# Kernel optimization log

Measured on AMD Instinct MI355X. Metric: run time of the kernel, lower is better.

The kernel has to match this reference:

```python
import jax, jax.numpy as jnp
import numpy as np

EPS_BN = 1e-5
EPS_LN = 1e-5


def conv2d(x, w, stride=1, padding=0):
    # x: [B,C,H,W], w: [O,I,kh,kw]
    return jax.lax.conv_general_dilated(
        x, w, (stride, stride), [(padding, padding), (padding, padding)],
        dimension_numbers=("NCHW", "OIHW", "NCHW"))


def bn_relu(x, g, b, m, v):
    inv = g / jnp.sqrt(v + EPS_BN)
    return jax.nn.relu(x * inv[None, :, None, None] + (b - m * inv)[None, :, None, None])


def haar_dwt(x):
    # orthonormal 2D Haar: [B,C,H,W] -> [B,4C,H/2,W/2] as concat(LL,LH,HL,HH)
    B, C, H, W = x.shape
    x = x.reshape(B, C, H // 2, 2, W // 2, 2)
    a = x[:, :, :, 0, :, 0]; b = x[:, :, :, 0, :, 1]
    c = x[:, :, :, 1, :, 0]; d = x[:, :, :, 1, :, 1]
    ll = (a + b + c + d) * 0.5
    lh = (a - b + c - d) * 0.5
    hl = (a + b - c - d) * 0.5
    hh = (a - b - c + d) * 0.5
    return jnp.concatenate([ll, lh, hl, hh], axis=1)


def haar_idwt(co):
    # exact inverse of haar_dwt: [B,4C,h,w] -> [B,C,2h,2w]
    B, C4, h, w = co.shape
    ll, lh, hl, hh = jnp.split(co, 4, axis=1)
    a = (ll + lh + hl + hh) * 0.5
    b = (ll - lh + hl - hh) * 0.5
    c = (ll + lh - hl - hh) * 0.5
    d = (ll - lh - hl + hh) * 0.5
    row0 = jnp.stack([a, b], axis=-1)  # [B,C,h,w,2]
    row1 = jnp.stack([c, d], axis=-1)
    y = jnp.stack([row0, row1], axis=3)  # [B,C,h,2,w,2]
    return y.reshape(B, C4 // 4, 2 * h, 2 * w)


def layernorm(x, g, b):
    mu = jnp.mean(x, axis=-1, keepdims=True)
    var = jnp.mean(jnp.square(x - mu), axis=-1, keepdims=True)
    return (x - mu) * jax.lax.rsqrt(var + EPS_LN) * g + b


def setup_inputs() -> dict:
    key = jax.random.key(0)
    ks = jax.random.split(key, 20)
    B, N, C = 16, 3136, 256
    red = C // 4  # 64
    sr = 2
    d = {}
    d["x"] = jax.random.normal(ks[0], (B, N, C), jnp.float32)
    d["height"] = 56
    d["width"] = 56
    # reduce: conv1x1 C->red (no bias) + BN
    d["reduce_w"] = jax.random.normal(ks[1], (red, C, 1, 1), jnp.float32) * 0.05
    d["bn1_g"] = jax.random.uniform(ks[2], (red,), jnp.float32, 0.5, 1.5)
    d["bn1_b"] = jax.random.normal(ks[3], (red,), jnp.float32) * 0.1
    d["bn1_m"] = jax.random.normal(ks[4], (red,), jnp.float32) * 0.1
    d["bn1_v"] = jax.random.uniform(ks[5], (red,), jnp.float32, 0.5, 1.5)
    # filter: conv3x3 C->C (no bias) + BN  (acts on 4*red = C coeff channels)
    d["filt_w"] = jax.random.normal(ks[6], (C, C, 3, 3), jnp.float32) * 0.02
    d["bn2_g"] = jax.random.uniform(ks[7], (C,), jnp.float32, 0.5, 1.5)
    d["bn2_b"] = jax.random.normal(ks[8], (C,), jnp.float32) * 0.1
    d["bn2_m"] = jax.random.normal(ks[9], (C,), jnp.float32) * 0.1
    d["bn2_v"] = jax.random.uniform(ks[10], (C,), jnp.float32, 0.5, 1.5)
    # kv_embed: conv kxk stride sr, C->C, with bias
    d["kve_w"] = jax.random.normal(ks[11], (C, C, sr, sr), jnp.float32) * 0.05
    d["kve_b"] = jnp.zeros((C,), jnp.float32)
    # q linear
    d["q_w"] = jax.random.normal(ks[12], (C, C), jnp.float32) * 0.05
    d["q_b"] = jnp.zeros((C,), jnp.float32)
    # kv layernorm + kv linear
    d["kvn_g"] = jnp.ones((C,), jnp.float32)
    d["kvn_b"] = jnp.zeros((C,), jnp.float32)
    d["kv_w"] = jax.random.normal(ks[13], (2 * C, C), jnp.float32) * 0.05
    d["kv_b"] = jnp.zeros((2 * C,), jnp.float32)
    # proj: (C + red) -> C
    d["proj_w"] = jax.random.normal(ks[14], (C, C + red), jnp.float32) * 0.05
    d["proj_b"] = jnp.zeros((C,), jnp.float32)
    return d


def reference(x, q_w, q_b, reduce_w, bn1_g, bn1_b, bn1_m, bn1_v,
              filt_w, bn2_g, bn2_b, bn2_m, bn2_v, kve_w, kve_b,
              kvn_g, kvn_b, kv_w, kv_b, proj_w, proj_b, height, width):
    B, N, C = x.shape
    H_heads, sr = 8, 2
    hd = C // H_heads
    scale = hd ** -0.5

    # queries [B,h,N,hd]
    q = (x @ q_w.T + q_b).reshape(B, N, H_heads, hd).transpose(0, 2, 1, 3)

    # spatial path
    spatial = x.transpose(0, 2, 1).reshape(B, C, height, width)
    reduced = bn_relu(conv2d(spatial, reduce_w), bn1_g, bn1_b, bn1_m, bn1_v)  # [B,C/4,H,W]
    coeffs = haar_dwt(reduced)  # [B,C,H/2,W/2]
    coeffs = bn_relu(conv2d(coeffs, filt_w, padding=1), bn2_g, bn2_b, bn2_m, bn2_v)
    local_context = haar_idwt(coeffs)  # [B,C/4,H,W]
    local_context = local_context.reshape(B, C // 4, N).transpose(0, 2, 1)  # [B,N,C/4]

    # kv path
    kv_src = conv2d(coeffs, kve_w, stride=sr) + kve_b[None, :, None, None]
    Bk, Ck, hk, wk = kv_src.shape
    kv_src = kv_src.reshape(B, C, hk * wk).transpose(0, 2, 1)  # [B,M,C]
    kv_src = layernorm(kv_src, kvn_g, kvn_b)
    kv = (kv_src @ kv_w.T + kv_b).reshape(B, -1, 2, H_heads, hd)
    kv = kv.transpose(2, 0, 3, 1, 4)  # [2,B,h,M,hd]
    key, value = kv[0], kv[1]

    # attention
    scores = jnp.einsum("bhnd,bhmd->bhnm", q, key) * scale
    probs = jax.nn.softmax(scores, axis=-1)
    attended = jnp.einsum("bhnm,bhmd->bhnd", probs, value)
    attended = attended.transpose(0, 2, 1, 3).reshape(B, N, C)

    out = jnp.concatenate([attended, local_context], axis=-1) @ proj_w.T + proj_b
    return out
```

## Files before the change

### kernel.cpp

```cpp
#include <hip/hip_runtime.h>
#include <hip/hip_bf16.h>
#include <math.h>


#define B_   16
#define NSP  3136
#define KVL  196
#define HD   32

typedef short bf16x8 __attribute__((ext_vector_type(8)));
typedef float f32x4  __attribute__((ext_vector_type(4)));

__device__ inline unsigned int f2bf(float f) {
    unsigned int u = __float_as_uint(f);
    u += 0x7FFFu + ((u >> 16) & 1u);
    return u >> 16;
}
__device__ inline float bf2f(unsigned short u) {
    return __uint_as_float(((unsigned int)u) << 16);
}
__device__ inline f32x4 max4(f32x4 a, f32x4 b) {
    f32x4 r;
    r[0] = fmaxf(a[0], b[0]); r[1] = fmaxf(a[1], b[1]);
    r[2] = fmaxf(a[2], b[2]); r[3] = fmaxf(a[3], b[3]);
    return r;
}

__global__ __launch_bounds__(256) void wcvt_k(
    const float* __restrict__ q, const float* __restrict__ red,
    const float* __restrict__ kv, const float* __restrict__ proj,
    unsigned short* __restrict__ dst)
{
    const int i = blockIdx.x * 256 + threadIdx.x;
    const int e = i * 4;
    const float* src; int off;
    if (e < 65536)       { src = q;    off = e; }
    else if (e < 81920)  { src = red;  off = e - 65536; }
    else if (e < 212992) { src = kv;   off = e - 81920; }
    else                 { src = proj; off = e - 212992; }
    const float4 v = *(const float4*)(src + off);
    const unsigned int p0 = f2bf(v.x) | (f2bf(v.y) << 16);
    const unsigned int p1 = f2bf(v.z) | (f2bf(v.w) << 16);
    *(uint2*)(dst + e) = make_uint2(p0, p1);
}

__global__ __launch_bounds__(256) void wcvt2_k(const float* __restrict__ kve,
                                               unsigned short* __restrict__ wk)
{
    const int i = blockIdx.x * 256 + threadIdx.x;
    const int n = i >> 8;
    const int rem = i & 255;
    const int tap = rem >> 6;
    const int ci0 = (rem & 63) * 4;
    const float* s = kve + (size_t)n * 1024;
    const unsigned int t0 = f2bf(s[(ci0 + 0) * 4 + tap]);
    const unsigned int t1 = f2bf(s[(ci0 + 1) * 4 + tap]);
    const unsigned int t2 = f2bf(s[(ci0 + 2) * 4 + tap]);
    const unsigned int t3 = f2bf(s[(ci0 + 3) * 4 + tap]);
    *(uint2*)(wk + (size_t)n * 1024 + tap * 256 + ci0) =
        make_uint2(t0 | (t1 << 16), t2 | (t3 << 16));
}

__global__ __launch_bounds__(256) void wcvt3_k(const float* __restrict__ filt,
                                               unsigned short* __restrict__ wf)
{
    const int i = blockIdx.x * 256 + threadIdx.x;
    const int n = i / 576;
    const int rem = (i - n * 576) * 4;
    const int tap = rem >> 8;
    const int ci = rem & 255;
    const float* s = filt + (size_t)n * 2304;
    const unsigned int t0 = f2bf(s[(ci + 0) * 9 + tap]);
    const unsigned int t1 = f2bf(s[(ci + 1) * 9 + tap]);
    const unsigned int t2 = f2bf(s[(ci + 2) * 9 + tap]);
    const unsigned int t3 = f2bf(s[(ci + 3) * 9 + tap]);
    *(uint2*)(wf + (size_t)n * 2304 + rem) = make_uint2(t0 | (t1 << 16), t2 | (t3 << 16));
}

template<int BM, int BN, int EPI, int LDM>
__global__ __launch_bounds__(256) void mgemm(
    const unsigned short* __restrict__ A, const float* __restrict__ Af,
    const unsigned short* __restrict__ Acl,
    const unsigned short* __restrict__ W, const float* __restrict__ bias,
    const float* __restrict__ g, const float* __restrict__ bb,
    const float* __restrict__ mm, const float* __restrict__ vv,
    float* __restrict__ out, float* __restrict__ out2,
    int Mpad, int Mvalid, int N, int K, float scale)
{
    constexpr int FM = BM / 32, FN = BN / 32;
    constexpr int RA = BM / 64, RB = BN / 64;
    __shared__ short As[BM][32];
    __shared__ short Bs[BN][32];
    const int tid = threadIdx.x, lane = tid & 63;
    const int w = tid >> 6, wr = w >> 1, wc = w & 1;
    const int b = blockIdx.z, m0 = blockIdx.x * BM, n0 = blockIdx.y * BN;
    const unsigned short* Ab = A + ((size_t)b * Mpad + m0) * (size_t)K;
    const unsigned short* Wb = W + (size_t)n0 * K;

    const int r_row0 = tid >> 2, kbase = (tid & 3) * 8;
    int ym[RA], xm[RA], mg[RA];
#pragma unroll
    for (int rnd = 0; rnd < RA; ++rnd) {
        const int m = m0 + rnd * 64 + r_row0;
        mg[rnd] = m;
        if constexpr (LDM == 1) { ym[rnd] = m / 28; xm[rnd] = m - 28 * ym[rnd]; }
        else if constexpr (LDM == 3) { ym[rnd] = m / 14; xm[rnd] = m - 14 * ym[rnd]; }
        else { ym[rnd] = 0; xm[rnd] = 0; }
    }

    f32x4 acc[FM][FN];
#pragma unroll
    for (int i = 0; i < FM; ++i)
#pragma unroll
        for (int j = 0; j < FN; ++j) acc[i][j] = (f32x4){0.f, 0.f, 0.f, 0.f};

    for (int k0 = 0; k0 < K; k0 += 32) {
#pragma unroll
        for (int rnd = 0; rnd < RA; ++rnd) {
            const int row = rnd * 64 + r_row0;
            if constexpr (LDM == 0) {
                *(int4*)&As[row][kbase] =
                    *(const int4*)(Ab + (size_t)row * K + k0 + kbase);
            } else if constexpr (LDM == 2) {
                unsigned int p0 = 0, p1 = 0, p2 = 0, p3 = 0;
                if (mg[rnd] < Mvalid) {
                    const float* sp = Af + ((size_t)b * Mvalid + mg[rnd]) * K + k0 + kbase;
                    const float4 v0 = *(const float4*)sp;
                    const float4 v1 = *(const float4*)(sp + 4);
                    p0 = f2bf(v0.x) | (f2bf(v0.y) << 16);
                    p1 = f2bf(v0.z) | (f2bf(v0.w) << 16);
                    p2 = f2bf(v1.x) | (f2bf(v1.y) << 16);
                    p3 = f2bf(v1.z) | (f2bf(v1.w) << 16);
                }
                *(int4*)&As[row][kbase] = make_int4(p0, p1, p2, p3);
            } else if constexpr (LDM == 1) {
                const int kk = k0 + kbase;
                const int tap = kk >> 8, ci0 = kk & 255;
                const int ky = tap / 3, kx = tap - 3 * ky;
                const int sy = ym[rnd] + ky - 1, sx = xm[rnd] + kx - 1;
                int4 v = make_int4(0, 0, 0, 0);
                if (mg[rnd] < Mvalid && sy >= 0 && sy < 28 && sx >= 0 && sx < 28)
                    v = *(const int4*)(Acl + ((size_t)b * 784 + sy * 28 + sx) * 256 + ci0);
                *(int4*)&As[row][kbase] = v;
            } else {
                const int kk = k0 + kbase;
                const int tap = kk >> 8, ci0 = kk & 255;
                const int ky = tap >> 1, kx = tap & 1;
                const int sy = 2 * ym[rnd] + ky, sx = 2 * xm[rnd] + kx;
                int4 v = make_int4(0, 0, 0, 0);
                if (mg[rnd] < Mvalid)
                    v = *(const int4*)(Acl + ((size_t)b * 784 + sy * 28 + sx) * 256 + ci0);
                *(int4*)&As[row][kbase] = v;
            }
        }
#pragma unroll
        for (int rnd = 0; rnd < RB; ++rnd) {
            const int row = rnd * 64 + r_row0;
            *(int4*)&Bs[row][kbase] =
                *(const int4*)(Wb + (size_t)row * K + k0 + kbase);
        }
        __syncthreads();
        bf16x8 af[FM], bfr[FN];
#pragma unroll
        for (int i = 0; i < FM; ++i)
            af[i] = *(const bf16x8*)&As[wr * (BM / 2) + i * 16 + (lane & 15)][(lane >> 4) * 8];
#pragma unroll
        for (int j = 0; j < FN; ++j)
            bfr[j] = *(const bf16x8*)&Bs[wc * (BN / 2) + j * 16 + (lane & 15)][(lane >> 4) * 8];
#pragma unroll
        for (int i = 0; i < FM; ++i)
#pragma unroll
            for (int j = 0; j < FN; ++j)
                acc[i][j] = __builtin_amdgcn_mfma_f32_16x16x32_bf16(af[i], bfr[j], acc[i][j], 0, 0, 0);
        __syncthreads();
    }

    const int cl = lane & 15, rh = lane >> 4;
#pragma unroll
    for (int i = 0; i < FM; ++i) {
#pragma unroll
        for (int j = 0; j < FN; ++j) {
            const int n = n0 + wc * (BN / 2) + j * 16 + cl;
#pragma unroll
            for (int r = 0; r < 4; ++r) {
                const int m = m0 + wr * (BM / 2) + i * 16 + rh * 4 + r;
                if (m >= Mvalid) continue;
                const float v = acc[i][j][r];
                if constexpr (EPI == 0) {
                    out[((size_t)b * Mvalid + m) * N + n] = v + bias[n];
                } else if constexpr (EPI == 1) {
                    unsigned short* qp = (unsigned short*)out;
                    const int h = (n >> 5) & 7, d = n & 31;
                    qp[(((size_t)b * 8 + h) * 3136 + m) * 32 + d] =
                        (unsigned short)f2bf((v + bias[n]) * scale);
                } else if constexpr (EPI == 3) {
                    const float val = v + bias[n];
                    const int h = (n >> 5) & 7, d = n & 31;
                    if (n < 256)
                        ((unsigned short*)out)[(((size_t)b * 8 + h) * 224 + m) * 32 + d] =
                            (unsigned short)f2bf(val);
                    else
                        ((unsigned short*)out2)[(((size_t)b * 8 + h) * 32 + d) * 224 + m] =
                            (unsigned short)f2bf(val);
                } else {
                    const float inv = g[n] * rsqrtf(vv[n] + 1e-5f);
                    const float rr = v * inv + (bb[n] - mm[n] * inv);
                    ((unsigned short*)out)[((size_t)b * Mvalid + m) * N + n] =
                        (unsigned short)f2bf(rr > 0.f ? rr : 0.f);
                }
            }
        }
    }
}

__global__ __launch_bounds__(256) void dwt_k(const unsigned short* __restrict__ rd,
                                             unsigned short* __restrict__ ccl)
{
    const int i = blockIdx.x * 256 + threadIdx.x;
    const int c4 = (i & 15) * 4;
    const int p = i >> 4;
    const int x = p % 28, y = (p / 28) % 28, b = p / 784;
    const unsigned short* ip = rd + ((size_t)b * 3136 + (2 * y) * 56 + 2 * x) * 64 + c4;
    const uint2 u00 = *(const uint2*)(ip);
    const uint2 u01 = *(const uint2*)(ip + 64);
    const uint2 u10 = *(const uint2*)(ip + 56 * 64);
    const uint2 u11 = *(const uint2*)(ip + 57 * 64);
    const unsigned short* s00 = (const unsigned short*)&u00;
    const unsigned short* s01 = (const unsigned short*)&u01;
    const unsigned short* s10 = (const unsigned short*)&u10;
    const unsigned short* s11 = (const unsigned short*)&u11;
    unsigned short ll[4], lh[4], hl[4], hh[4];
#pragma unroll
    for (int j = 0; j < 4; ++j) {
        const float a = bf2f(s00[j]), bq = bf2f(s01[j]);
        const float c = bf2f(s10[j]), d = bf2f(s11[j]);
        ll[j] = (unsigned short)f2bf((a + bq + c + d) * 0.5f);
        lh[j] = (unsigned short)f2bf((a - bq + c - d) * 0.5f);
        hl[j] = (unsigned short)f2bf((a + bq - c - d) * 0.5f);
        hh[j] = (unsigned short)f2bf((a - bq - c + d) * 0.5f);
    }
    unsigned short* op = ccl + ((size_t)b * 784 + y * 28 + x) * 256 + c4;
    *(uint2*)(op)       = make_uint2(ll[0] | (ll[1] << 16), ll[2] | (ll[3] << 16));
    *(uint2*)(op + 64)  = make_uint2(lh[0] | (lh[1] << 16), lh[2] | (lh[3] << 16));
    *(uint2*)(op + 128) = make_uint2(hl[0] | (hl[1] << 16), hl[2] | (hl[3] << 16));
    *(uint2*)(op + 192) = make_uint2(hh[0] | (hh[1] << 16), hh[2] | (hh[3] << 16));
}

__global__ __launch_bounds__(256) void idwt_k(const unsigned short* __restrict__ c2,
                                              unsigned short* __restrict__ aproj)
{
    const int i = blockIdx.x * 256 + threadIdx.x;
    const int c4 = (i & 15) * 4;
    const int p = i >> 4;
    const int m = p % 3136, b = p / 3136;
    const int Y = m / 56, X = m - 56 * Y;
    const int y = Y >> 1, x = X >> 1;
    const unsigned short* ip = c2 + ((size_t)b * 784 + y * 28 + x) * 256 + c4;
    const uint2 ull = *(const uint2*)(ip);
    const uint2 ulh = *(const uint2*)(ip + 64);
    const uint2 uhl = *(const uint2*)(ip + 128);
    const uint2 uhh = *(const uint2*)(ip + 192);
    const unsigned short* sll = (const unsigned short*)&ull;
    const unsigned short* slh = (const unsigned short*)&ulh;
    const unsigned short* shl = (const unsigned short*)&uhl;
    const unsigned short* shh = (const unsigned short*)&uhh;
    const float flh = (X & 1) ? -0.5f : 0.5f;
    const float fhl = (Y & 1) ? -0.5f : 0.5f;
    const float fhh = ((X ^ Y) & 1) ? -0.5f : 0.5f;
    unsigned short o[4];
#pragma unroll
    for (int j = 0; j < 4; ++j) {
        const float v = 0.5f * bf2f(sll[j]) + flh * bf2f(slh[j]) +
                        fhl * bf2f(shl[j]) + fhh * bf2f(shh[j]);
        o[j] = (unsigned short)f2bf(v);
    }
    *(uint2*)(aproj + ((size_t)b * 3200 + m) * 320 + 256 + c4) =
        make_uint2(o[0] | (o[1] << 16), o[2] | (o[3] << 16));
}

__global__ __launch_bounds__(256) void ln_k(const float* __restrict__ in,
                                            const float* __restrict__ g,
                                            const float* __restrict__ bb,
                                            unsigned short* __restrict__ outp)
{
    const int rg = blockIdx.x;
    const int rl = rg & 255, b = rg >> 8;
    const int t = threadIdx.x;
    unsigned short* op = outp + (size_t)rg * 256 + t;
    if (rl >= 196) { *op = 0; return; }
    const float x = in[((size_t)(b * 196) + rl) * 256 + t];
    __shared__ float r1[4], r2[4];
    float s = x;
#pragma unroll
    for (int o = 32; o > 0; o >>= 1) s += __shfl_down(s, o);
    if ((t & 63) == 0) r1[t >> 6] = s;
    __syncthreads();
    const float mu = (r1[0] + r1[1] + r1[2] + r1[3]) * (1.f / 256.f);
    const float d = x - mu;
    float s2 = d * d;
#pragma unroll
    for (int o = 32; o > 0; o >>= 1) s2 += __shfl_down(s2, o);
    if ((t & 63) == 0) r2[t >> 6] = s2;
    __syncthreads();
    const float var = (r2[0] + r2[1] + r2[2] + r2[3]) * (1.f / 256.f);
    *op = (unsigned short)f2bf(d * rsqrtf(var + 1e-5f) * g[t] + bb[t]);
}

__global__ __launch_bounds__(256) void attn_m(
    const unsigned short* __restrict__ qb, const unsigned short* __restrict__ kb,
    const unsigned short* __restrict__ vt, unsigned short* __restrict__ aproj)
{
    __shared__ short Pl[4][16][232];
    const int tid = threadIdx.x, lane = tid & 63, w = tid >> 6;
    const int bh = blockIdx.y, b = bh >> 3, h = bh & 7;
    const int q0 = blockIdx.x * 64 + w * 16;
    const int cl = lane & 15, hi = lane >> 4;

    const bf16x8 qf = *(const bf16x8*)(qb + ((size_t)bh * 3136 + q0 + cl) * 32 + hi * 8);

    f32x4 s[13];
    const unsigned short* kp = kb + (size_t)bh * 224 * 32;
#pragma unroll
    for (int t = 0; t < 13; ++t) {
        const bf16x8 kf = *(const bf16x8*)(kp + (size_t)(t * 16 + cl) * 32 + hi * 8);
        s[t] = __builtin_amdgcn_mfma_f32_16x16x32_bf16(kf, qf,
                                                       (f32x4){0.f, 0.f, 0.f, 0.f}, 0, 0, 0);
    }
    if (hi) s[12] = (f32x4){-1e30f, -1e30f, -1e30f, -1e30f};

    f32x4 t0 = max4(s[0], s[1]), t1 = max4(s[2], s[3]), t2 = max4(s[4], s[5]);
    f32x4 t3 = max4(s[6], s[7]), t4 = max4(s[8], s[9]), t5 = max4(s[10], s[11]);
    t0 = max4(t0, t1); t2 = max4(t2, t3); t4 = max4(t4, s[12]);
    t0 = max4(t0, t2); t0 = max4(t0, max4(t4, t5));
    float m = fmaxf(fmaxf(t0[0], t0[1]), fmaxf(t0[2], t0[3]));
    m = fmaxf(m, __shfl_xor(m, 16));
    m = fmaxf(m, __shfl_xor(m, 32));

#pragma unroll
    for (int t = 0; t < 13; ++t) {
#pragma unroll
        for (int r = 0; r < 4; ++r) s[t][r] = exp2f(s[t][r] - m);
    }

    short* prow = &Pl[w][cl][0];
#pragma unroll
    for (int t = 0; t < 13; ++t) {
        __hip_bfloat162 pa = __float22bfloat162_rn(make_float2(s[t][0], s[t][1]));
        __hip_bfloat162 pb = __float22bfloat162_rn(make_float2(s[t][2], s[t][3]));
        unsigned int ua, ub;
        __builtin_memcpy(&ua, &pa, 4);
        __builtin_memcpy(&ub, &pb, 4);
        *(uint2*)(prow + t * 16 + hi * 4) = make_uint2(ua, ub);
    }
    *(uint2*)(prow + 208 + hi * 4) = make_uint2(0u, 0u);

    bf16x8 onesf;
#pragma unroll
    for (int j = 0; j < 8; ++j) onesf[j] = (short)0x3F80;
    f32x4 o0 = (f32x4){0.f, 0.f, 0.f, 0.f};
    f32x4 o1 = (f32x4){0.f, 0.f, 0.f, 0.f};
    f32x4 osum = (f32x4){0.f, 0.f, 0.f, 0.f};
    const unsigned short* vp0 = vt + ((size_t)bh * 32 + cl) * 224;
    const unsigned short* vp1 = vp0 + 16 * 224;
#pragma unroll
    for (int kk = 0; kk < 7; ++kk) {
        const bf16x8 pf = *(const bf16x8*)(prow + kk * 32 + hi * 8);
        const bf16x8 v0 = *(const bf16x8*)(vp0 + kk * 32 + hi * 8);
        const bf16x8 v1 = *(const bf16x8*)(vp1 + kk * 32 + hi * 8);
        o0 = __builtin_amdgcn_mfma_f32_16x16x32_bf16(pf, v0, o0, 0, 0, 0);
        o1 = __builtin_amdgcn_mfma_f32_16x16x32_bf16(pf, v1, o1, 0, 0, 0);
        osum = __builtin_amdgcn_mfma_f32_16x16x32_bf16(pf, onesf, osum, 0, 0, 0);
    }

    float* ol = (float*)&Pl[w][0][0];
#pragma unroll
    for (int r = 0; r < 4; ++r) {
        const float rq = __builtin_amdgcn_rcpf(osum[r]);
        ol[(hi * 4 + r) * 36 + cl]      = o0[r] * rq;
        ol[(hi * 4 + r) * 36 + cl + 16] = o1[r] * rq;
    }
    const int row = lane >> 2, c8 = (lane & 3) * 8;
    const float4 b0 = *(const float4*)(ol + row * 36 + c8);
    const float4 b1 = *(const float4*)(ol + row * 36 + c8 + 4);
    __hip_bfloat162 pa = __float22bfloat162_rn(make_float2(b0.x, b0.y));
    __hip_bfloat162 pb = __float22bfloat162_rn(make_float2(b0.z, b0.w));
    __hip_bfloat162 pc = __float22bfloat162_rn(make_float2(b1.x, b1.y));
    __hip_bfloat162 pd = __float22bfloat162_rn(make_float2(b1.z, b1.w));
    unsigned int k0, k1, k2, k3;
    __builtin_memcpy(&k0, &pa, 4);
    __builtin_memcpy(&k1, &pb, 4);
    __builtin_memcpy(&k2, &pc, 4);
    __builtin_memcpy(&k3, &pd, 4);
    *(uint4*)(aproj + ((size_t)b * 3200 + q0 + row) * 320 + h * 32 + c8) =
        make_uint4(k0, k1, k2, k3);
}

extern "C" void kernel_launch(void* const* d_in, const int* in_sizes, int n_in,
                              void* d_out, int out_size, void* d_ws, size_t ws_size,
                              hipStream_t stream)
{
    const float* x        = (const float*)d_in[0];
    const float* reduce_w = (const float*)d_in[3];
    const float* bn1_g    = (const float*)d_in[4];
    const float* bn1_b    = (const float*)d_in[5];
    const float* bn1_m    = (const float*)d_in[6];
    const float* bn1_v    = (const float*)d_in[7];
    const float* filt_w   = (const float*)d_in[8];
    const float* bn2_g    = (const float*)d_in[9];
    const float* bn2_b    = (const float*)d_in[10];
    const float* bn2_m    = (const float*)d_in[11];
    const float* bn2_v    = (const float*)d_in[12];
    const float* kve_w    = (const float*)d_in[13];
    const float* kve_b    = (const float*)d_in[14];
    const float* q_w      = (const float*)d_in[15];
    const float* q_b      = (const float*)d_in[16];
    const float* kvn_g    = (const float*)d_in[17];
    const float* kvn_b    = (const float*)d_in[18];
    const float* kv_w     = (const float*)d_in[19];
    const float* kv_b     = (const float*)d_in[20];
    const float* proj_w   = (const float*)d_in[21];
    const float* proj_b   = (const float*)d_in[22];

    float* out = (float*)d_out;
    float* ws  = (float*)d_ws;

    unsigned short* aproj = (unsigned short*)ws;
    unsigned short* rd_cl = (unsigned short*)(ws +  8192000);
    unsigned short* ccl   = (unsigned short*)(ws +  9797632);
    unsigned short* ccl2  = (unsigned short*)(ws + 11403264);
    float* kv_src         = ws + 13008896;
    unsigned short* kbuf  = (unsigned short*)(ws + 13811712);
    unsigned short* vtb   = (unsigned short*)(ws + 14270464);
    unsigned short* kv_ln = (unsigned short*)(ws + 14729216);
    unsigned short* wpl   = (unsigned short*)(ws + 15253504);
    unsigned short* wkve  = (unsigned short*)(ws + 15400960);
    unsigned short* wfilt = (unsigned short*)(ws + 15532032);
    unsigned short* wq    = wpl;
    unsigned short* wred  = wpl + 65536;
    unsigned short* wkv   = wpl + 81920;
    unsigned short* wproj = wpl + 212992;
    unsigned short* qb    = (unsigned short*)d_out;

    const float scale = 0.17677669529663689f * 1.4426950408889634f;

    wcvt_k<<<288, 256, 0, stream>>>(q_w, reduce_w, kv_w, proj_w, wpl);
    wcvt2_k<<<256, 256, 0, stream>>>(kve_w, wkve);
    wcvt3_k<<<576, 256, 0, stream>>>(filt_w, wfilt);

    mgemm<128, 128, 1, 2><<<dim3(25, 2, B_), 256, 0, stream>>>(
        nullptr, x, nullptr, wq, q_b, nullptr, nullptr, nullptr, nullptr,
        out, nullptr, 3136, 3136, 256, 256, scale);

    mgemm<128, 64, 4, 2><<<dim3(25, 1, B_), 256, 0, stream>>>(
        nullptr, x, nullptr, wred, nullptr, bn1_g, bn1_b, bn1_m, bn1_v,
        (float*)rd_cl, nullptr, 3136, 3136, 64, 256, 0.f);

    dwt_k<<<784, 256, 0, stream>>>(rd_cl, ccl);

    mgemm<64, 64, 4, 1><<<dim3(13, 4, B_), 256, 0, stream>>>(
        nullptr, nullptr, ccl, wfilt, nullptr, bn2_g, bn2_b, bn2_m, bn2_v,
        (float*)ccl2, nullptr, 832, 784, 256, 2304, 0.f);

    idwt_k<<<3136, 256, 0, stream>>>(ccl2, aproj);

    mgemm<64, 64, 0, 3><<<dim3(4, 4, B_), 256, 0, stream>>>(
        nullptr, nullptr, ccl2, wkve, kve_b, nullptr, nullptr, nullptr, nullptr,
        kv_src, nullptr, 256, 196, 256, 1024, 0.f);

    ln_k<<<4096, 256, 0, stream>>>(kv_src, kvn_g, kvn_b, kv_ln);

    mgemm<64, 128, 3, 0><<<dim3(4, 4, B_), 256, 0, stream>>>(
        kv_ln, nullptr, nullptr, wkv, kv_b, nullptr, nullptr, nullptr, nullptr,
        (float*)kbuf, (float*)vtb, 256, 196, 512, 256, 0.f);

    attn_m<<<dim3(49, 128), 256, 0, stream>>>(qb, kbuf, vtb, aproj);

    mgemm<128, 128, 0, 0><<<dim3(25, 2, B_), 256, 0, stream>>>(
        aproj, nullptr, nullptr, wproj, proj_b, nullptr, nullptr, nullptr, nullptr,
        out, nullptr, 3200, 3136, 256, 320, 0.f);
}
```

Measured before the change: 261.8 us.

## Merge weight conversion kernels and process two query tiles per attention wave

The three weight-conversion kernels become one launch that dispatches on block index, saving two kernel launches. The attention kernel now has each wave handle two 16-row query groups, which halves the grid and amortizes per-block setup. It also switches to the raw exp2 builtin and adds an occupancy hint to launch bounds. Because 3136 is not a multiple of 128, the last block has idle waves that exit early.

```diff
diff --git a/kernel.cpp b/kernel.cpp
--- a/kernel.cpp
+++ b/kernel.cpp
@@ -26,55 +26,53 @@
     return r;
 }
 
-__global__ __launch_bounds__(256) void wcvt_k(
+__global__ __launch_bounds__(256) void wall_k(
     const float* __restrict__ q, const float* __restrict__ red,
     const float* __restrict__ kv, const float* __restrict__ proj,
-    unsigned short* __restrict__ dst)
-{
-    const int i = blockIdx.x * 256 + threadIdx.x;
-    const int e = i * 4;
-    const float* src; int off;
-    if (e < 65536)       { src = q;    off = e; }
-    else if (e < 81920)  { src = red;  off = e - 65536; }
-    else if (e < 212992) { src = kv;   off = e - 81920; }
-    else                 { src = proj; off = e - 212992; }
-    const float4 v = *(const float4*)(src + off);
-    const unsigned int p0 = f2bf(v.x) | (f2bf(v.y) << 16);
-    const unsigned int p1 = f2bf(v.z) | (f2bf(v.w) << 16);
-    *(uint2*)(dst + e) = make_uint2(p0, p1);
-}
-
-__global__ __launch_bounds__(256) void wcvt2_k(const float* __restrict__ kve,
-                                               unsigned short* __restrict__ wk)
-{
-    const int i = blockIdx.x * 256 + threadIdx.x;
-    const int n = i >> 8;
-    const int rem = i & 255;
-    const int tap = rem >> 6;
-    const int ci0 = (rem & 63) * 4;
-    const float* s = kve + (size_t)n * 1024;
-    const unsigned int t0 = f2bf(s[(ci0 + 0) * 4 + tap]);
-    const unsigned int t1 = f2bf(s[(ci0 + 1) * 4 + tap]);
-    const unsigned int t2 = f2bf(s[(ci0 + 2) * 4 + tap]);
-    const unsigned int t3 = f2bf(s[(ci0 + 3) * 4 + tap]);
-    *(uint2*)(wk + (size_t)n * 1024 + tap * 256 + ci0) =
-        make_uint2(t0 | (t1 << 16), t2 | (t3 << 16));
-}
-
-__global__ __launch_bounds__(256) void wcvt3_k(const float* __restrict__ filt,
-                                               unsigned short* __restrict__ wf)
-{
-    const int i = blockIdx.x * 256 + threadIdx.x;
-    const int n = i / 576;
-    const int rem = (i - n * 576) * 4;
-    const int tap = rem >> 8;
-    const int ci = rem & 255;
-    const float* s = filt + (size_t)n * 2304;
-    const unsigned int t0 = f2bf(s[(ci + 0) * 9 + tap]);
-    const unsigned int t1 = f2bf(s[(ci + 1) * 9 + tap]);
-    const unsigned int t2 = f2bf(s[(ci + 2) * 9 + tap]);
-    const unsigned int t3 = f2bf(s[(ci + 3) * 9 + tap]);
-    *(uint2*)(wf + (size_t)n * 2304 + rem) = make_uint2(t0 | (t1 << 16), t2 | (t3 << 16));
+    const float* __restrict__ kve, const float* __restrict__ filt,
+    unsigned short* __restrict__ wpl, unsigned short* __restrict__ wkve,
+    unsigned short* __restrict__ wfilt)
+{
+    const int bid = blockIdx.x;
+    if (bid < 288) {
+        const int i = bid * 256 + threadIdx.x;
+        const int e = i * 4;
+        const float* src; int off;
+        if (e < 65536)       { src = q;    off = e; }
+        else if (e < 81920)  { src = red;  off = e - 65536; }
+        else if (e < 212992) { src = kv;   off = e - 81920; }
+        else                 { src = proj; off = e - 212992; }
+        const float4 v = *(const float4*)(src + off);
+        const unsigned int p0 = f2bf(v.x) | (f2bf(v.y) << 16);
+        const unsigned int p1 = f2bf(v.z) | (f2bf(v.w) << 16);
+        *(uint2*)(wpl + e) = make_uint2(p0, p1);
+    } else if (bid < 544) {
+        const int i = (bid - 288) * 256 + threadIdx.x;
+        const int n = i >> 8;
+        const int rem = i & 255;
+        const int tap = rem >> 6;
+        const int ci0 = (rem & 63) * 4;
+        const float* s = kve + (size_t)n * 1024;
+        const unsigned int t0 = f2bf(s[(ci0 + 0) * 4 + tap]);
+        const unsigned int t1 = f2bf(s[(ci0 + 1) * 4 + tap]);
+        const unsigned int t2 = f2bf(s[(ci0 + 2) * 4 + tap]);
+        const unsigned int t3 = f2bf(s[(ci0 + 3) * 4 + tap]);
+        *(uint2*)(wkve + (size_t)n * 1024 + tap * 256 + ci0) =
+            make_uint2(t0 | (t1 << 16), t2 | (t3 << 16));
+    } else {
+        const int i = (bid - 544) * 256 + threadIdx.x;
+        const int n = i / 576;
+        const int rem = (i - n * 576) * 4;
+        const int tap = rem >> 8;
+        const int ci = rem & 255;
+        const float* s = filt + (size_t)n * 2304;
+        const unsigned int t0 = f2bf(s[(ci + 0) * 9 + tap]);
+        const unsigned int t1 = f2bf(s[(ci + 1) * 9 + tap]);
+        const unsigned int t2 = f2bf(s[(ci + 2) * 9 + tap]);
+        const unsigned int t3 = f2bf(s[(ci + 3) * 9 + tap]);
+        *(uint2*)(wfilt + (size_t)n * 2304 + rem) =
+            make_uint2(t0 | (t1 << 16), t2 | (t3 << 16));
+    }
 }
 
 template<int BM, int BN, int EPI, int LDM>
@@ -306,93 +304,99 @@
     *op = (unsigned short)f2bf(d * rsqrtf(var + 1e-5f) * g[t] + bb[t]);
 }
 
-__global__ __launch_bounds__(256) void attn_m(
+__global__ __launch_bounds__(256, 4) void attn_m(
     const unsigned short* __restrict__ qb, const unsigned short* __restrict__ kb,
     const unsigned short* __restrict__ vt, unsigned short* __restrict__ aproj)
 {
     __shared__ short Pl[4][16][232];
     const int tid = threadIdx.x, lane = tid & 63, w = tid >> 6;
     const int bh = blockIdx.y, b = bh >> 3, h = bh & 7;
-    const int q0 = blockIdx.x * 64 + w * 16;
+    const int q0w = blockIdx.x * 128 + w * 32;
+    if (q0w >= NSP) return;
     const int cl = lane & 15, hi = lane >> 4;
-
-    const bf16x8 qf = *(const bf16x8*)(qb + ((size_t)bh * 3136 + q0 + cl) * 32 + hi * 8);
-
-    f32x4 s[13];
     const unsigned short* kp = kb + (size_t)bh * 224 * 32;
-#pragma unroll
-    for (int t = 0; t < 13; ++t) {
-        const bf16x8 kf = *(const bf16x8*)(kp + (size_t)(t * 16 + cl) * 32 + hi * 8);
-        s[t] = __builtin_amdgcn_mfma_f32_16x16x32_bf16(kf, qf,
-                                                       (f32x4){0.f, 0.f, 0.f, 0.f}, 0, 0, 0);
-    }
-    if (hi) s[12] = (f32x4){-1e30f, -1e30f, -1e30f, -1e30f};
-
-    f32x4 t0 = max4(s[0], s[1]), t1 = max4(s[2], s[3]), t2 = max4(s[4], s[5]);
-    f32x4 t3 = max4(s[6], s[7]), t4 = max4(s[8], s[9]), t5 = max4(s[10], s[11]);
-    t0 = max4(t0, t1); t2 = max4(t2, t3); t4 = max4(t4, s[12]);
-    t0 = max4(t0, t2); t0 = max4(t0, max4(t4, t5));
-    float m = fmaxf(fmaxf(t0[0], t0[1]), fmaxf(t0[2], t0[3]));
-    m = fmaxf(m, __shfl_xor(m, 16));
-    m = fmaxf(m, __shfl_xor(m, 32));
-
-#pragma unroll
-    for (int t = 0; t < 13; ++t) {
-#pragma unroll
-        for (int r = 0; r < 4; ++r) s[t][r] = exp2f(s[t][r] - m);
-    }
-
-    short* prow = &Pl[w][cl][0];
-#pragma unroll
-    for (int t = 0; t < 13; ++t) {
-        __hip_bfloat162 pa = __float22bfloat162_rn(make_float2(s[t][0], s[t][1]));
-        __hip_bfloat162 pb = __float22bfloat162_rn(make_float2(s[t][2], s[t][3]));
-        unsigned int ua, ub;
-        __builtin_memcpy(&ua, &pa, 4);
-        __builtin_memcpy(&ub, &pb, 4);
-        *(uint2*)(prow + t * 16 + hi * 4) = make_uint2(ua, ub);
-    }
-    *(uint2*)(prow + 208 + hi * 4) = make_uint2(0u, 0u);
-
-    bf16x8 onesf;
-#pragma unroll
-    for (int j = 0; j < 8; ++j) onesf[j] = (short)0x3F80;
-    f32x4 o0 = (f32x4){0.f, 0.f, 0.f, 0.f};
-    f32x4 o1 = (f32x4){0.f, 0.f, 0.f, 0.f};
-    f32x4 osum = (f32x4){0.f, 0.f, 0.f, 0.f};
     const unsigned short* vp0 = vt + ((size_t)bh * 32 + cl) * 224;
     const unsigned short* vp1 = vp0 + 16 * 224;
-#pragma unroll
-    for (int kk = 0; kk < 7; ++kk) {
-        const bf16x8 pf = *(const bf16x8*)(prow + kk * 32 + hi * 8);
-        const bf16x8 v0 = *(const bf16x8*)(vp0 + kk * 32 + hi * 8);
-        const bf16x8 v1 = *(const bf16x8*)(vp1 + kk * 32 + hi * 8);
-        o0 = __builtin_amdgcn_mfma_f32_16x16x32_bf16(pf, v0, o0, 0, 0, 0);
-        o1 = __builtin_amdgcn_mfma_f32_16x16x32_bf16(pf, v1, o1, 0, 0, 0);
-        osum = __builtin_amdgcn_mfma_f32_16x16x32_bf16(pf, onesf, osum, 0, 0, 0);
-    }
-
+    short* prow = &Pl[w][cl][0];
     float* ol = (float*)&Pl[w][0][0];
-#pragma unroll
-    for (int r = 0; r < 4; ++r) {
-        const float rq = __builtin_amdgcn_rcpf(osum[r]);
-        ol[(hi * 4 + r) * 36 + cl]      = o0[r] * rq;
-        ol[(hi * 4 + r) * 36 + cl + 16] = o1[r] * rq;
-    }
+    bf16x8 onesf;
+#pragma unroll
+    for (int j = 0; j < 8; ++j) onesf[j] = (short)0x3F80;
     const int row = lane >> 2, c8 = (lane & 3) * 8;
-    const float4 b0 = *(const float4*)(ol + row * 36 + c8);
-    const float4 b1 = *(const float4*)(ol + row * 36 + c8 + 4);
-    __hip_bfloat162 pa = __float22bfloat162_rn(make_float2(b0.x, b0.y));
-    __hip_bfloat162 pb = __float22bfloat162_rn(make_float2(b0.z, b0.w));
-    __hip_bfloat162 pc = __float22bfloat162_rn(make_float2(b1.x, b1.y));
-    __hip_bfloat162 pd = __float22bfloat162_rn(make_float2(b1.z, b1.w));
-    unsigned int k0, k1, k2, k3;
-    __builtin_memcpy(&k0, &pa, 4);
-    __builtin_memcpy(&k1, &pb, 4);
-    __builtin_memcpy(&k2, &pc, 4);
-    __builtin_memcpy(&k3, &pd, 4);
-    *(uint4*)(aproj + ((size_t)b * 3200 + q0 + row) * 320 + h * 32 + c8) =
-        make_uint4(k0, k1, k2, k3);
+
+#pragma unroll
+    for (int g = 0; g < 2; ++g) {
+        const int q0 = q0w + g * 16;
+        const bf16x8 qf = *(const bf16x8*)(qb + ((size_t)bh * 3136 + q0 + cl) * 32 + hi * 8);
+
+        f32x4 s[13];
+#pragma unroll
+        for (int t = 0; t < 13; ++t) {
+            const bf16x8 kf = *(const bf16x8*)(kp + (size_t)(t * 16 + cl) * 32 + hi * 8);
+            s[t] = __builtin_amdgcn_mfma_f32_16x16x32_bf16(kf, qf,
+                                                           (f32x4){0.f, 0.f, 0.f, 0.f}, 0, 0, 0);
+        }
+        if (hi) s[12] = (f32x4){-1e30f, -1e30f, -1e30f, -1e30f};
+
+        f32x4 t0 = max4(s[0], s[1]), t1 = max4(s[2], s[3]), t2 = max4(s[4], s[5]);
+        f32x4 t3 = max4(s[6], s[7]), t4 = max4(s[8], s[9]), t5 = max4(s[10], s[11]);
+        t0 = max4(t0, t1); t2 = max4(t2, t3); t4 = max4(t4, s[12]);
+        t0 = max4(t0, t2); t0 = max4(t0, max4(t4, t5));
+        float m = fmaxf(fmaxf(t0[0], t0[1]), fmaxf(t0[2], t0[3]));
+        m = fmaxf(m, __shfl_xor(m, 16));
+        m = fmaxf(m, __shfl_xor(m, 32));
+
+#pragma unroll
+        for (int t = 0; t < 13; ++t) {
+#pragma unroll
+            for (int r = 0; r < 4; ++r)
+                s[t][r] = __builtin_amdgcn_exp2f(s[t][r] - m);
+        }
+
+#pragma unroll
+        for (int t = 0; t < 13; ++t) {
+            __hip_bfloat162 pa = __float22bfloat162_rn(make_float2(s[t][0], s[t][1]));
+            __hip_bfloat162 pb = __float22bfloat162_rn(make_float2(s[t][2], s[t][3]));
+            unsigned int ua, ub;
+            __builtin_memcpy(&ua, &pa, 4);
+            __builtin_memcpy(&ub, &pb, 4);
+            *(uint2*)(prow + t * 16 + hi * 4) = make_uint2(ua, ub);
+        }
+        *(uint2*)(prow + 208 + hi * 4) = make_uint2(0u, 0u);
+
+        f32x4 o0 = (f32x4){0.f, 0.f, 0.f, 0.f};
+        f32x4 o1 = (f32x4){0.f, 0.f, 0.f, 0.f};
+        f32x4 osum = (f32x4){0.f, 0.f, 0.f, 0.f};
+#pragma unroll
+        for (int kk = 0; kk < 7; ++kk) {
+            const bf16x8 pf = *(const bf16x8*)(prow + kk * 32 + hi * 8);
+            const bf16x8 v0 = *(const bf16x8*)(vp0 + kk * 32 + hi * 8);
+            const bf16x8 v1 = *(const bf16x8*)(vp1 + kk * 32 + hi * 8);
+            o0 = __builtin_amdgcn_mfma_f32_16x16x32_bf16(pf, v0, o0, 0, 0, 0);
+            o1 = __builtin_amdgcn_mfma_f32_16x16x32_bf16(pf, v1, o1, 0, 0, 0);
+            osum = __builtin_amdgcn_mfma_f32_16x16x32_bf16(pf, onesf, osum, 0, 0, 0);
+        }
+
+#pragma unroll
+        for (int r = 0; r < 4; ++r) {
+            const float rq = __builtin_amdgcn_rcpf(osum[r]);
+            ol[(hi * 4 + r) * 36 + cl]      = o0[r] * rq;
+            ol[(hi * 4 + r) * 36 + cl + 16] = o1[r] * rq;
+        }
+        const float4 b0 = *(const float4*)(ol + row * 36 + c8);
+        const float4 b1 = *(const float4*)(ol + row * 36 + c8 + 4);
+        __hip_bfloat162 pa = __float22bfloat162_rn(make_float2(b0.x, b0.y));
+        __hip_bfloat162 pb = __float22bfloat162_rn(make_float2(b0.z, b0.w));
+        __hip_bfloat162 pc = __float22bfloat162_rn(make_float2(b1.x, b1.y));
+        __hip_bfloat162 pd = __float22bfloat162_rn(make_float2(b1.z, b1.w));
+        unsigned int k0, k1, k2, k3;
+        __builtin_memcpy(&k0, &pa, 4);
+        __builtin_memcpy(&k1, &pb, 4);
+        __builtin_memcpy(&k2, &pc, 4);
+        __builtin_memcpy(&k3, &pd, 4);
+        *(uint4*)(aproj + ((size_t)b * 3200 + q0 + row) * 320 + h * 32 + c8) =
+            make_uint4(k0, k1, k2, k3);
+    }
 }
 
 extern "C" void kernel_launch(void* const* d_in, const int* in_sizes, int n_in,
@@ -443,9 +447,8 @@
 
     const float scale = 0.17677669529663689f * 1.4426950408889634f;
 
-    wcvt_k<<<288, 256, 0, stream>>>(q_w, reduce_w, kv_w, proj_w, wpl);
-    wcvt2_k<<<256, 256, 0, stream>>>(kve_w, wkve);
-    wcvt3_k<<<576, 256, 0, stream>>>(filt_w, wfilt);
+    wall_k<<<1120, 256, 0, stream>>>(q_w, reduce_w, kv_w, proj_w, kve_w, filt_w,
+                                     wpl, wkve, wfilt);
 
     mgemm<128, 128, 1, 2><<<dim3(25, 2, B_), 256, 0, stream>>>(
         nullptr, x, nullptr, wq, q_b, nullptr, nullptr, nullptr, nullptr,
@@ -473,7 +476,7 @@
         kv_ln, nullptr, nullptr, wkv, kv_b, nullptr, nullptr, nullptr, nullptr,
         (float*)kbuf, (float*)vtb, 256, 196, 512, 256, 0.f);
 
-    attn_m<<<dim3(49, 128), 256, 0, stream>>>(qb, kbuf, vtb, aproj);
+    attn_m<<<dim3(25, 128), 256, 0, stream>>>(qb, kbuf, vtb, aproj);
 
     mgemm<128, 128, 0, 0><<<dim3(25, 2, B_), 256, 0, stream>>>(
         aproj, nullptr, nullptr, wproj, proj_b, nullptr, nullptr, nullptr, nullptr,
```

Measured after the change: 251.6 us. -3.9%, faster.
